# Performance work log

Measured on AMD Instinct MI355X. Metric: run time of the kernel, lower is better.

## Reference

```python
import jax, jax.numpy as jnp
import numpy as np

B, T, NUM_IN, H, O = 64, 128, 256, 512, 256
BANKS, N, M = 4, 128, 64
R = BANKS * N  # addressable memory rows (flattened over banks)
EPS = 1e-8


def _lin(key, out_d, in_d):
    s = 1.0 / np.sqrt(in_d)
    kw, kb = jax.random.split(key)
    W = jax.random.uniform(kw, (out_d, in_d), jnp.float32, -s, s)
    b = jax.random.uniform(kb, (out_d,), jnp.float32, -s, s)
    return W, b


def setup_inputs() -> dict:
    key = jax.random.key(0)
    ks = jax.random.split(key, 16)
    inp = {
        "x": jax.random.normal(ks[0], (B, T, 16, 16), jnp.float32),
        "h": jnp.zeros((B, H), jnp.float32),
        "frf": jnp.full((B, R), 1.0 / R, jnp.float32),
        "wrf": jnp.full((B, R), 1.0 / R, jnp.float32),
        "fwf": jnp.full((B, R), 1.0 / R, jnp.float32),
        "wwf": jnp.full((B, R), 1.0 / R, jnp.float32),
        "m": 0.1 * jax.random.normal(ks[1], (B, BANKS, N, M), jnp.float32),
    }
    inp["W_in"], inp["b_in"] = _lin(ks[2], H, NUM_IN)
    inp["W_read"], inp["b_read"] = _lin(ks[3], H, M)
    inp["W_out"], inp["b_out"] = _lin(ks[4], O, H)
    inp["W_kr"], inp["b_kr"] = _lin(ks[5], M, H)
    inp["W_br"], inp["b_br"] = _lin(ks[6], 1, H)
    inp["W_gr"], inp["b_gr"] = _lin(ks[7], 1, H)
    inp["W_kw"], inp["b_kw"] = _lin(ks[8], M, H)
    inp["W_bw"], inp["b_bw"] = _lin(ks[9], 1, H)
    inp["W_gw"], inp["b_gw"] = _lin(ks[10], 1, H)
    inp["W_e"], inp["b_e"] = _lin(ks[11], M, H)
    inp["W_a"], inp["b_a"] = _lin(ks[12], M, H)
    return inp


def _smooth(w):
    # wide filter: circular 3-tap blur of the focused filter over memory rows
    return 0.25 * jnp.roll(w, 1, axis=-1) + 0.5 * w + 0.25 * jnp.roll(w, -1, axis=-1)


def _address(h, mem2, f_prev, W_k, b_k, W_b, b_b, W_g, b_g):
    # content-based addressing with focused/wide filter pair (NTM-style)
    k = jnp.tanh(h @ W_k.T + b_k)                                  # [B,M]
    beta = jax.nn.softplus(h @ W_b.T + b_b)                        # [B,1]
    g = jax.nn.sigmoid(h @ W_g.T + b_g)                            # [B,1]
    dots = jnp.einsum("bm,brm->br", k, mem2)
    denom = (jnp.linalg.norm(k, axis=-1, keepdims=True)
             * jnp.linalg.norm(mem2, axis=-1) + EPS)
    wc = jax.nn.softmax(beta * dots / denom, axis=-1)              # [B,R]
    f_new = g * wc + (1.0 - g) * f_prev                            # focused filter
    w_new = _smooth(f_new)                                         # wide filter
    return f_new, w_new, 0.5 * (f_new + w_new)


def reference(x, h, frf, wrf, fwf, wwf, m,
              W_in, b_in, W_read, b_read, W_out, b_out,
              W_kr, b_kr, W_br, b_br, W_gr, b_gr,
              W_kw, b_kw, W_bw, b_bw, W_gw, b_gw,
              W_e, b_e, W_a, b_a):
    xs = x.transpose(1, 0, 2, 3).reshape(T, B, -1)  # [T,B,NUM_IN]

    def step(carry, x_t):
        h_t, frf_t, wrf_t, fwf_t, wwf_t, m_t = carry
        mem2 = m_t.reshape(B, R, M)
        # --- EMM read ---
        frf_n, wrf_n, w_read = _address(h_t, mem2, frf_t,
                                        W_kr, b_kr, W_br, b_br, W_gr, b_gr)
        r_t = jnp.einsum("br,brm->bm", w_read, mem2)               # [B,M]
        # --- EMM write ---
        fwf_n, wwf_n, w_write = _address(h_t, mem2, fwf_t,
                                         W_kw, b_kw, W_bw, b_bw, W_gw, b_gw)
        e = jax.nn.sigmoid(h_t @ W_e.T + b_e)                      # erase [B,M]
        a = jnp.tanh(h_t @ W_a.T + b_a)                            # add   [B,M]
        mem_new = (mem2 * (1.0 - w_write[:, :, None] * e[:, None, :])
                   + w_write[:, :, None] * a[:, None, :])
        m_n = mem_new.reshape(B, BANKS, N, M)
        # --- controller + output ---
        h_n = jax.nn.relu(x_t @ W_in.T + b_in + r_t @ W_read.T + b_read)
        out = jax.nn.sigmoid(h_n @ W_out.T + b_out)                # [B,O]
        return (h_n, frf_n, wrf_n, fwf_n, wwf_n, m_n), out

    _, outs = jax.lax.scan(step, (h, frf, wrf, fwf, wwf, m), xs)
    return outs.transpose(1, 0, 2)  # [B,T,O]
```

## Files before the change

### kernel.cpp

```cpp
#include <hip/hip_runtime.h>
#include <math.h>

#define B_   64
#define T_   128
#define NIN  256
#define H_   512
#define O_   256
#define M_   64
#define R_   512
#define EPS_ 1e-8f

typedef _Float16 h2 __attribute__((ext_vector_type(2)));

__device__ __forceinline__ float dot4(float4 a, float4 b) {
    return a.x*b.x + a.y*b.y + a.z*b.z + a.w*b.w;
}

__device__ __forceinline__ float frcp(float x) {
#if __has_builtin(__builtin_amdgcn_rcpf)
    return __builtin_amdgcn_rcpf(x);
#else
    return 1.f / x;
#endif
}
__device__ __forceinline__ float fsqrt_(float x) {
#if __has_builtin(__builtin_amdgcn_sqrtf)
    return __builtin_amdgcn_sqrtf(x);
#else
    return sqrtf(x);
#endif
}

__device__ __forceinline__ float fd2(unsigned wu, unsigned hu, float acc) {
#if __has_builtin(__builtin_amdgcn_fdot2)
    return __builtin_amdgcn_fdot2(__builtin_bit_cast(h2, wu),
                                  __builtin_bit_cast(h2, hu), acc, false);
#else
    h2 w = __builtin_bit_cast(h2, wu), h = __builtin_bit_cast(h2, hu);
    return acc + (float)w[0]*(float)h[0] + (float)w[1]*(float)h[1];
#endif
}
#define FD4(W, HX, A) { A = fd2(W.x, HX.x, A); A = fd2(W.y, HX.y, A); \
                        A = fd2(W.z, HX.z, A); A = fd2(W.w, HX.w, A); }

__device__ __forceinline__ unsigned pk16(float a, float b) {
    return __builtin_bit_cast(unsigned, __builtin_amdgcn_cvt_pkrtz(a, b));
}
__device__ __forceinline__ unsigned short bits16(float v) {
    return __builtin_bit_cast(unsigned short, (_Float16)v);
}

template<int CTRL>
__device__ __forceinline__ float dpp_add(float v) {
    int t = __builtin_amdgcn_update_dpp(0, __float_as_int(v), CTRL, 0xF, 0xF, false);
    return v + __int_as_float(t);
}
template<int CTRL>
__device__ __forceinline__ float dpp_mov(float v) {
    return __int_as_float(__builtin_amdgcn_update_dpp(0, __float_as_int(v), CTRL, 0xF, 0xF, false));
}
__device__ __forceinline__ float red16(float v) {
    v = dpp_add<0xB1>(v);
    v = dpp_add<0x4E>(v);
    v = dpp_add<0x124>(v);
    v = dpp_add<0x128>(v);
    return v;
}
__device__ __forceinline__ float red64_pair(float v) {
    v = dpp_add<0x4E>(v);
    v = dpp_add<0x124>(v);
    v = dpp_add<0x128>(v);
    v += __shfl_xor(v, 16, 64);
    v += __shfl_xor(v, 32, 64);
    return v;
}
__device__ __forceinline__ float sigmoid_f(float x) { return frcp(1.f + __expf(-x)); }
__device__ __forceinline__ float softplus_f(float x){ return x > 20.f ? x : log1pf(__expf(x)); }

__global__ __launch_bounds__(256) void w2h(
    const float* __restrict__ Wkr, const float* __restrict__ Wkw,
    const float* __restrict__ We,  const float* __restrict__ Wa,
    const float* __restrict__ Wbr, const float* __restrict__ Wgr,
    const float* __restrict__ Wbw, const float* __restrict__ Wgw,
    unsigned short* __restrict__ Wh)
{
    if (blockIdx.x == 128) {
        const int idx = threadIdx.x * 8;
        #pragma unroll
        for (int k = 0; k < 8; ++k) {
            int i2 = idx + k;
            int mi2 = i2 >> 9;
            const float* s2 = mi2 == 0 ? Wbr : mi2 == 1 ? Wgr : mi2 == 2 ? Wbw : Wgw;
            Wh[256 * H_ + i2] = bits16(s2[i2 & (H_ - 1)]);
        }
        return;
    }
    const int mi = blockIdx.x >> 5;
    const float* s = mi == 0 ? Wkr : mi == 1 ? Wkw : mi == 2 ? We : Wa;
    const int off = (blockIdx.x & 31) * 1024 + threadIdx.x * 4;
    float4 v = *(const float4*)&s[off];
    ushort4 o;
    o.x = bits16(v.x); o.y = bits16(v.y); o.z = bits16(v.z); o.w = bits16(v.w);
    *(ushort4*)&Wh[mi * 32768 + off] = o;
}

__global__ __launch_bounds__(256) void xin_gemm(
    const float* __restrict__ x, const float* __restrict__ Win,
    const float* __restrict__ bin, unsigned short* __restrict__ xin_h)
{
    __shared__ __align__(16) float xs[32 * NIN];
    const int tid  = threadIdx.x;
    const int row0 = blockIdx.x * 32;

    #pragma unroll
    for (int i = 0; i < 8; ++i) {
        int idx = i * 1024 + tid * 4;
        *(float4*)&xs[idx] = *(const float4*)&x[(size_t)row0 * NIN + idx];
    }
    __syncthreads();

    const int rg = tid >> 6;
    const int cg = tid & 63;
    const int c0 = cg * 8;
    float acc[8][8];
    #pragma unroll
    for (int r = 0; r < 8; ++r)
        #pragma unroll
        for (int c = 0; c < 8; ++c) acc[r][c] = 0.f;

    for (int k = 0; k < NIN; k += 4) {
        float4 xq[8];
        #pragma unroll
        for (int r = 0; r < 8; ++r) xq[r] = *(float4*)&xs[(rg * 8 + r) * NIN + k];
        #pragma unroll
        for (int c = 0; c < 8; ++c) {
            float4 w4 = *(const float4*)&Win[(size_t)(c0 + c) * NIN + k];
            #pragma unroll
            for (int r = 0; r < 8; ++r) acc[r][c] += dot4(xq[r], w4);
        }
    }
    #pragma unroll
    for (int r = 0; r < 8; ++r) {
        int grow = row0 + rg * 8 + r;
        ushort4 o0, o1;
        o0.x = bits16(acc[r][0] + bin[c0 + 0]);
        o0.y = bits16(acc[r][1] + bin[c0 + 1]);
        o0.z = bits16(acc[r][2] + bin[c0 + 2]);
        o0.w = bits16(acc[r][3] + bin[c0 + 3]);
        o1.x = bits16(acc[r][4] + bin[c0 + 4]);
        o1.y = bits16(acc[r][5] + bin[c0 + 5]);
        o1.z = bits16(acc[r][6] + bin[c0 + 6]);
        o1.w = bits16(acc[r][7] + bin[c0 + 7]);
        *(ushort4*)&xin_h[(size_t)grow * H_ + c0]     = o0;
        *(ushort4*)&xin_h[(size_t)grow * H_ + c0 + 4] = o1;
    }
}

__global__ __launch_bounds__(512, 2) void ntm_loop(
    const unsigned short* __restrict__ xin_h,
    const float* __restrict__ h0,
    const float* __restrict__ frf0, const float* __restrict__ fwf0,
    const float* __restrict__ m0,
    const unsigned short* __restrict__ Wh,
    const float* __restrict__ bkr_g, const float* __restrict__ bkw_g,
    const float* __restrict__ be_g,  const float* __restrict__ ba_g,
    const float* __restrict__ bbr_g, const float* __restrict__ bgr_g,
    const float* __restrict__ bbw_g, const float* __restrict__ bgw_g,
    const float* __restrict__ Wread, const float* __restrict__ bread_g,
    float* __restrict__ h_all)
{
    __shared__ __align__(16) unsigned short hh40[16 * 40];
    __shared__ __align__(16) unsigned wrh[R_ * 36];
    __shared__ __align__(16) float2 ffb[2][R_];
    __shared__ __align__(16) float2 dotsRW[R_];
    __shared__ __align__(16) float2 fwp[R_];
    __shared__ __align__(16) float proj4[4 * M_];
    __shared__ __align__(16) float rtp[8][M_];
    __shared__ __align__(16) float rt8[8][M_];
    __shared__ __align__(16) float2 wsumRW[16];
    __shared__ __align__(16) float bias256[4 * M_];
    __shared__ __align__(16) unsigned wheadu[4 * H_ / 2];
    __shared__ float bhead[4];
    __shared__ float scal[4];

    const int b    = blockIdx.x;
    const int tid  = threadIdx.x;
    const int wave = tid >> 6, lane = tid & 63;
    const int g    = lane >> 4, sub = lane & 15;
    const int group = tid >> 4, s16 = tid & 15;

    const float* mg = m0 + (size_t)b * (R_ * M_);
    float4 mreg[16];
    #pragma unroll
    for (int i = 0; i < 16; ++i)
        mreg[i] = *(const float4*)&mg[(wave * 64 + i * 4 + g) * M_ + sub * 4];

    uint4 w16[32];
    #pragma unroll
    for (int p = 0; p < 8; ++p)
        #pragma unroll
        for (int j = 0; j < 4; ++j)
            w16[p * 4 + j] = *(const uint4*)&Wh[(size_t)(p * 32 + group) * H_ + s16 * 32 + j * 8];

    hh40[(tid >> 5) * 40 + (tid & 31)] = bits16(h0[b * H_ + tid]);
    ffb[0][tid] = make_float2(frf0[b * R_ + tid], fwf0[b * R_ + tid]);
    if (tid < M_) {
        bias256[tid]          = bkr_g[tid];
        bias256[M_ + tid]     = bkw_g[tid];
        bias256[2 * M_ + tid] = be_g[tid];
        bias256[3 * M_ + tid] = ba_g[tid];
    }
    if (tid >= 8 && tid < 16) wsumRW[tid] = make_float2(0.f, 0.f);
    wheadu[tid * 2]     = ((const unsigned*)&Wh[256 * H_])[tid * 2];
    wheadu[tid * 2 + 1] = ((const unsigned*)&Wh[256 * H_])[tid * 2 + 1];
    if (tid < 4) bhead[tid] = (tid == 0 ? bbr_g : tid == 1 ? bgr_g : tid == 2 ? bbw_g : bgw_g)[0];

    {
        const float* wrp = Wread + (size_t)tid * M_;
        #pragma unroll
        for (int wd = 0; wd < 2; ++wd)
            #pragma unroll
            for (int c = 0; c < 4; ++c) {
                float4 wa = *(const float4*)&wrp[wd * 32 + c * 8];
                float4 wb = *(const float4*)&wrp[wd * 32 + c * 8 + 4];
                uint4 o;
                o.x = pk16(wa.x, wa.y); o.y = pk16(wa.z, wa.w);
                o.z = pk16(wb.x, wb.y); o.w = pk16(wb.z, wb.w);
                *(uint4*)&wrh[tid * 36 + wd * 16 + c * 4] = o;
            }
    }
    const float breg = bread_g[tid];
    __syncthreads();

    for (int t = 0; t < T_; ++t) {
        const int cur = t & 1, nxt = cur ^ 1;

        unsigned short xbits = xin_h[(size_t)(b * T_ + t) * H_ + tid];
        {
            uint4 hx0 = *(const uint4*)&hh40[s16 * 40 + 0];
            uint4 hx1 = *(const uint4*)&hh40[s16 * 40 + 8];
            uint4 hx2 = *(const uint4*)&hh40[s16 * 40 + 16];
            uint4 hx3 = *(const uint4*)&hh40[s16 * 40 + 24];
            float a[8];
            #pragma unroll
            for (int p = 0; p < 8; ++p) {
                float acc = 0.f;
                FD4(w16[p * 4 + 0], hx0, acc);
                FD4(w16[p * 4 + 1], hx1, acc);
                FD4(w16[p * 4 + 2], hx2, acc);
                FD4(w16[p * 4 + 3], hx3, acc);
                a[p] = red16(acc);
            }
            float av = a[0];
            #pragma unroll
            for (int p = 1; p < 8; ++p) av = (s16 == p) ? a[p] : av;
            const int rowp = (s16 & 7) * 32 + group;
            const int m = rowp >> 6;
            float xv = av + bias256[rowp];
            float e  = __expf((m == 2) ? -xv : 2.f * xv);
            float rcp = frcp(1.f + e);
            float act = (m == 2) ? rcp : 1.f - 2.f * rcp;
            if (s16 < 8) proj4[rowp] = act;

            if (wave == 0) {
                float a8 = 0.f;
                uint4 wh0 = *(const uint4*)&wheadu[group * 256 + s16 * 16 + 0];
                uint4 wh1 = *(const uint4*)&wheadu[group * 256 + s16 * 16 + 4];
                uint4 wh2 = *(const uint4*)&wheadu[group * 256 + s16 * 16 + 8];
                uint4 wh3 = *(const uint4*)&wheadu[group * 256 + s16 * 16 + 12];
                FD4(wh0, hx0, a8); FD4(wh1, hx1, a8);
                FD4(wh2, hx2, a8); FD4(wh3, hx3, a8);
                a8 = red16(a8);
                if (s16 == 0) {
                    float hv = a8 + bhead[group];
                    scal[group] = (group & 1) ? sigmoid_f(hv) : softplus_f(hv);
                }
            }
        }
        __syncthreads();

        {
            float4 kr4 = *(float4*)&proj4[sub * 4];
            float4 kw4 = *(float4*)&proj4[M_ + sub * 4];
            float snKR = fsqrt_(red16(dot4(kr4, kr4)));
            float snKW = fsqrt_(red16(dot4(kw4, kw4)));
            const bool isW = (sub == 1);
            float bta = isW ? scal[2] : scal[0];
            float snK = isW ? snKW : snKR;
            float eacc = 0.f;
            #pragma unroll
            for (int i = 0; i < 16; ++i) {
                int r = wave * 64 + i * 4 + g;
                float4 v = mreg[i];
                float c = dot4(kr4, v);
                float d = dot4(kw4, v);
                float n = dot4(v, v);
                float c2 = dpp_add<0xB1>(c), d2 = dpp_add<0xB1>(d), n2 = dpp_add<0xB1>(n);
                float c4 = dpp_add<0x4E>(c2), d4 = dpp_add<0x4E>(d2), n4 = dpp_add<0x4E>(n2);
                const int q = sub & 3;
                float z = (q == 0) ? c4 : (q == 1 ? d4 : n4);
                z = dpp_add<0x124>(z);
                z = dpp_add<0x128>(z);
                float nt = dpp_mov<0xAA>(z);
                float sn = fsqrt_(nt);
                float ee = __expf(bta * z * frcp(snK * sn + EPS_));
                float eo = dpp_mov<0xB1>(ee);
                if (sub == 0) dotsRW[r] = make_float2(ee, eo);
                eacc += (sub < 2) ? ee : 0.f;
            }
            float vsum = red64_pair(eacc);
            float vo = dpp_mov<0xB1>(vsum);
            if (lane == 0) wsumRW[wave] = make_float2(vsum, vo);
        }
        __syncthreads();

        {
            float2 ws = wsumRW[lane & 15];
            float totR = red16(ws.x);
            float totW = red16(ws.y);
            {
                const int r = wave * 64 + lane;
                float invR = frcp(totR), invW = frcp(totW);
                const int rm = (r + R_ - 1) & (R_ - 1), rp = (r + 1) & (R_ - 1);
                float gr = scal[1], gw = scal[3];
                float2 d0 = dotsRW[r];
                float2 dm = dotsRW[rm];
                float2 dp = dotsRW[rp];
                float2 p0 = ffb[cur][r];
                float2 pm = ffb[cur][rm];
                float2 pp = ffb[cur][rp];

                float f0 = gr * d0.x * invR + (1.f - gr) * p0.x;
                float fm = gr * dm.x * invR + (1.f - gr) * pm.x;
                float fp = gr * dp.x * invR + (1.f - gr) * pp.x;
                float q0 = gw * d0.y * invW + (1.f - gw) * p0.y;
                float qm = gw * dm.y * invW + (1.f - gw) * pm.y;
                float qp = gw * dp.y * invW + (1.f - gw) * pp.y;
                ffb[nxt][r] = make_float2(f0, q0);
                fwp[r] = make_float2(0.75f * f0 + 0.125f * (fm + fp),
                                     0.75f * q0 + 0.125f * (qm + qp));
            }
            __builtin_amdgcn_wave_barrier();

            float2 fw2[16];
            #pragma unroll
            for (int i = 0; i < 16; ++i)
                fw2[i] = fwp[wave * 64 + i * 4 + g];

            float4 e4 = *(float4*)&proj4[2 * M_ + sub * 4];
            float4 a4 = *(float4*)&proj4[3 * M_ + sub * 4];
            float rt0 = 0, rt1 = 0, rt2 = 0, rt3 = 0;
            #pragma unroll
            for (int i = 0; i < 16; ++i) {
                float wr = fw2[i].x, ww = fw2[i].y;
                float4 v = mreg[i];
                rt0 += wr * v.x; rt1 += wr * v.y; rt2 += wr * v.z; rt3 += wr * v.w;
                float4 nv;
                nv.x = v.x * (1.f - ww * e4.x) + ww * a4.x;
                nv.y = v.y * (1.f - ww * e4.y) + ww * a4.y;
                nv.z = v.z * (1.f - ww * e4.z) + ww * a4.z;
                nv.w = v.w * (1.f - ww * e4.w) + ww * a4.w;
                mreg[i] = nv;
            }
            rt0 += __shfl_xor(rt0, 16, 64); rt0 += __shfl_xor(rt0, 32, 64);
            rt1 += __shfl_xor(rt1, 16, 64); rt1 += __shfl_xor(rt1, 32, 64);
            rt2 += __shfl_xor(rt2, 16, 64); rt2 += __shfl_xor(rt2, 32, 64);
            rt3 += __shfl_xor(rt3, 16, 64); rt3 += __shfl_xor(rt3, 32, 64);
            if (g == 0)
                *(float4*)&rtp[wave][sub * 4] = make_float4(rt0, rt1, rt2, rt3);
        }
        __syncthreads();

        {
            float rsum = rtp[0][lane] + rtp[1][lane] + rtp[2][lane] + rtp[3][lane]
                       + rtp[4][lane] + rtp[5][lane] + rtp[6][lane] + rtp[7][lane];
            rt8[wave][lane] = rsum;
            __builtin_amdgcn_wave_barrier();

            float acc = 0.f;
            #pragma unroll
            for (int wd = 0; wd < 2; ++wd)
                #pragma unroll
                for (int c = 0; c < 4; ++c) {
                    uint4 wq = *(uint4*)&wrh[tid * 36 + wd * 16 + c * 4];
                    float4 ra = *(float4*)&rt8[wave][wd * 32 + c * 8];
                    float4 rb = *(float4*)&rt8[wave][wd * 32 + c * 8 + 4];
                    unsigned p0 = pk16(ra.x, ra.y), p1 = pk16(ra.z, ra.w);
                    unsigned p2 = pk16(rb.x, rb.y), p3 = pk16(rb.z, rb.w);
                    acc = fd2(wq.x, p0, acc); acc = fd2(wq.y, p1, acc);
                    acc = fd2(wq.z, p2, acc); acc = fd2(wq.w, p3, acc);
                }
            float xv = (float)__builtin_bit_cast(_Float16, xbits);
            float hv = fmaxf(xv + acc + breg, 0.f);
            hh40[(tid >> 5) * 40 + (tid & 31)] = bits16(hv);
            h_all[(size_t)(b * T_ + t) * H_ + tid] = hv;
        }
        __syncthreads();
    }
}

__global__ __launch_bounds__(256) void out_gemm(
    const float* __restrict__ h_all, const float* __restrict__ Wout,
    const float* __restrict__ bout, float* __restrict__ out)
{
    __shared__ __align__(16) float hs[32 * H_];
    const int tid  = threadIdx.x;
    const int row0 = blockIdx.x * 32;

    #pragma unroll
    for (int i = 0; i < 16; ++i) {
        int idx = i * 1024 + tid * 4;
        *(float4*)&hs[idx] = *(const float4*)&h_all[(size_t)row0 * H_ + idx];
    }
    __syncthreads();

    const int rg = tid >> 6;
    const int cg = tid & 63;
    const int c0 = cg * 4;
    float acc[8][4];
    #pragma unroll
    for (int r = 0; r < 8; ++r)
        #pragma unroll
        for (int c = 0; c < 4; ++c) acc[r][c] = 0.f;

    for (int k = 0; k < H_; k += 4) {
        float4 xq[8];
        #pragma unroll
        for (int r = 0; r < 8; ++r) xq[r] = *(float4*)&hs[(rg * 8 + r) * H_ + k];
        #pragma unroll
        for (int c = 0; c < 4; ++c) {
            float4 w4 = *(const float4*)&Wout[(size_t)(c0 + c) * H_ + k];
            #pragma unroll
            for (int r = 0; r < 8; ++r) acc[r][c] += dot4(xq[r], w4);
        }
    }
    #pragma unroll
    for (int r = 0; r < 8; ++r) {
        int grow = row0 + rg * 8 + r;
        float4 o4;
        o4.x = sigmoid_f(acc[r][0] + bout[c0 + 0]);
        o4.y = sigmoid_f(acc[r][1] + bout[c0 + 1]);
        o4.z = sigmoid_f(acc[r][2] + bout[c0 + 2]);
        o4.w = sigmoid_f(acc[r][3] + bout[c0 + 3]);
        *(float4*)&out[(size_t)grow * O_ + c0] = o4;
    }
}

extern "C" void kernel_launch(void* const* d_in, const int* in_sizes, int n_in,
                              void* d_out, int out_size, void* d_ws, size_t ws_size,
                              hipStream_t stream) {
    const float* x     = (const float*)d_in[0];
    const float* h0    = (const float*)d_in[1];
    const float* frf   = (const float*)d_in[2];
    const float* fwf   = (const float*)d_in[4];
    const float* m0    = (const float*)d_in[6];
    const float* Win   = (const float*)d_in[7];
    const float* bin   = (const float*)d_in[8];
    const float* Wread = (const float*)d_in[9];
    const float* bread = (const float*)d_in[10];
    const float* Wout  = (const float*)d_in[11];
    const float* bout  = (const float*)d_in[12];
    const float* Wkr   = (const float*)d_in[13];
    const float* bkr   = (const float*)d_in[14];
    const float* Wbr   = (const float*)d_in[15];
    const float* bbr   = (const float*)d_in[16];
    const float* Wgr   = (const float*)d_in[17];
    const float* bgr   = (const float*)d_in[18];
    const float* Wkw   = (const float*)d_in[19];
    const float* bkw   = (const float*)d_in[20];
    const float* Wbw   = (const float*)d_in[21];
    const float* bbw   = (const float*)d_in[22];
    const float* Wgw   = (const float*)d_in[23];
    const float* bgw   = (const float*)d_in[24];
    const float* We    = (const float*)d_in[25];
    const float* be    = (const float*)d_in[26];
    const float* Wa    = (const float*)d_in[27];
    const float* ba    = (const float*)d_in[28];

    unsigned short* xin_h = (unsigned short*)d_ws;
    float* h_all = (float*)((char*)d_ws + (size_t)B_ * T_ * H_ * 2);
    unsigned short* Wh = (unsigned short*)((char*)d_ws + (size_t)B_ * T_ * H_ * 6);

    w2h<<<129, 256, 0, stream>>>(Wkr, Wkw, We, Wa, Wbr, Wgr, Wbw, Wgw, Wh);
    xin_gemm<<<256, 256, 0, stream>>>(x, Win, bin, xin_h);
    ntm_loop<<<B_, 512, 0, stream>>>(xin_h, h0, frf, fwf, m0,
        Wh, bkr, bkw, be, ba,
        bbr, bgr, bbw, bgw,
        Wread, bread, h_all);
    out_gemm<<<256, 256, 0, stream>>>(h_all, Wout, bout, (float*)d_out);
}
```

Before: 900.9 us.

## Replace input and output FP32 GEMMs with FP16 MFMA matrix-core kernels

Adds a conversion kernel that casts x, W_in and W_out to half precision, then replaces the scalar FP32 xin and out GEMMs with one generic MFMA 16x16x32 f16 GEMM kernel. The recurrent loop now writes its hidden states in half precision instead of FP32, which halves that traffic and feeds the output GEMM directly. The goal is to move the two large batched GEMMs onto matrix cores. In exchange it adds an extra conversion pass over x, loses precision in h and x, and reads A and B straight from global memory without LDS staging.

```diff
diff --git a/kernel.cpp b/kernel.cpp
--- a/kernel.cpp
+++ b/kernel.cpp
@@ -11,6 +11,8 @@
 #define EPS_ 1e-8f
 
 typedef _Float16 h2 __attribute__((ext_vector_type(2)));
+typedef _Float16 f16x8 __attribute__((ext_vector_type(8)));
+typedef float f32x4 __attribute__((ext_vector_type(4)));
 
 __device__ __forceinline__ float dot4(float4 a, float4 b) {
     return a.x*b.x + a.y*b.y + a.z*b.z + a.w*b.w;
@@ -76,6 +78,23 @@
 }
 __device__ __forceinline__ float sigmoid_f(float x) { return frcp(1.f + __expf(-x)); }
 __device__ __forceinline__ float softplus_f(float x){ return x > 20.f ? x : log1pf(__expf(x)); }
+
+__global__ __launch_bounds__(256) void cvt_all(
+    const float* __restrict__ x, const float* __restrict__ Win,
+    const float* __restrict__ Wout,
+    unsigned short* __restrict__ xh, unsigned short* __restrict__ Winh,
+    unsigned short* __restrict__ Wouth)
+{
+    const int bid = blockIdx.x;
+    const float* src; unsigned short* dst; int idx;
+    if (bid < 2048)      { src = x;    dst = xh;    idx = bid * 1024 + threadIdx.x * 4; }
+    else if (bid < 2176) { src = Win;  dst = Winh;  idx = (bid - 2048) * 1024 + threadIdx.x * 4; }
+    else                 { src = Wout; dst = Wouth; idx = (bid - 2176) * 1024 + threadIdx.x * 4; }
+    float4 v = *(const float4*)&src[idx];
+    ushort4 o;
+    o.x = bits16(v.x); o.y = bits16(v.y); o.z = bits16(v.z); o.w = bits16(v.w);
+    *(ushort4*)&dst[idx] = o;
+}
 
 __global__ __launch_bounds__(256) void w2h(
     const float* __restrict__ Wkr, const float* __restrict__ Wkw,
@@ -104,55 +123,48 @@
     *(ushort4*)&Wh[mi * 32768 + off] = o;
 }
 
-__global__ __launch_bounds__(256) void xin_gemm(
-    const float* __restrict__ x, const float* __restrict__ Win,
-    const float* __restrict__ bin, unsigned short* __restrict__ xin_h)
+__global__ __launch_bounds__(256) void gemm_mfma(
+    const unsigned short* __restrict__ Ah, const unsigned short* __restrict__ Bh,
+    const float* __restrict__ bias, void* __restrict__ outp,
+    int M, int K, int N, int mode)
 {
-    __shared__ __align__(16) float xs[32 * NIN];
     const int tid  = threadIdx.x;
-    const int row0 = blockIdx.x * 32;
-
+    const int wv   = tid >> 6, lane = tid & 63;
+    const int m0   = blockIdx.x * 128 + wv * 32;
+    const int n0   = blockIdx.y * 64;
+    const int fr   = lane & 15, kg = lane >> 4;
+
+    f32x4 acc[2][4] = {};
+    const unsigned short* pa0 = Ah + (size_t)(m0 + fr) * K + kg * 8;
+    const unsigned short* pa1 = pa0 + (size_t)16 * K;
+    const unsigned short* pb  = Bh + (size_t)(n0 + fr) * K + kg * 8;
+
+    for (int k0 = 0; k0 < K; k0 += 32) {
+        f16x8 a0 = *(const f16x8*)(pa0 + k0);
+        f16x8 a1 = *(const f16x8*)(pa1 + k0);
+        #pragma unroll
+        for (int j = 0; j < 4; ++j) {
+            f16x8 bj = *(const f16x8*)(pb + (size_t)j * 16 * K + k0);
+            acc[0][j] = __builtin_amdgcn_mfma_f32_16x16x32_f16(a0, bj, acc[0][j], 0, 0, 0);
+            acc[1][j] = __builtin_amdgcn_mfma_f32_16x16x32_f16(a1, bj, acc[1][j], 0, 0, 0);
+        }
+    }
     #pragma unroll
-    for (int i = 0; i < 8; ++i) {
-        int idx = i * 1024 + tid * 4;
-        *(float4*)&xs[idx] = *(const float4*)&x[(size_t)row0 * NIN + idx];
-    }
-    __syncthreads();
-
-    const int rg = tid >> 6;
-    const int cg = tid & 63;
-    const int c0 = cg * 8;
-    float acc[8][8];
-    #pragma unroll
-    for (int r = 0; r < 8; ++r)
+    for (int j = 0; j < 4; ++j) {
+        const int gcol = n0 + j * 16 + fr;
+        const float bv = bias[gcol];
         #pragma unroll
-        for (int c = 0; c < 8; ++c) acc[r][c] = 0.f;
-
-    for (int k = 0; k < NIN; k += 4) {
-        float4 xq[8];
-        #pragma unroll
-        for (int r = 0; r < 8; ++r) xq[r] = *(float4*)&xs[(rg * 8 + r) * NIN + k];
-        #pragma unroll
-        for (int c = 0; c < 8; ++c) {
-            float4 w4 = *(const float4*)&Win[(size_t)(c0 + c) * NIN + k];
-            #pragma unroll
-            for (int r = 0; r < 8; ++r) acc[r][c] += dot4(xq[r], w4);
-        }
-    }
-    #pragma unroll
-    for (int r = 0; r < 8; ++r) {
-        int grow = row0 + rg * 8 + r;
-        ushort4 o0, o1;
-        o0.x = bits16(acc[r][0] + bin[c0 + 0]);
-        o0.y = bits16(acc[r][1] + bin[c0 + 1]);
-        o0.z = bits16(acc[r][2] + bin[c0 + 2]);
-        o0.w = bits16(acc[r][3] + bin[c0 + 3]);
-        o1.x = bits16(acc[r][4] + bin[c0 + 4]);
-        o1.y = bits16(acc[r][5] + bin[c0 + 5]);
-        o1.z = bits16(acc[r][6] + bin[c0 + 6]);
-        o1.w = bits16(acc[r][7] + bin[c0 + 7]);
-        *(ushort4*)&xin_h[(size_t)grow * H_ + c0]     = o0;
-        *(ushort4*)&xin_h[(size_t)grow * H_ + c0 + 4] = o1;
+        for (int i = 0; i < 2; ++i) {
+            #pragma unroll
+            for (int r = 0; r < 4; ++r) {
+                const int grow = m0 + i * 16 + kg * 4 + r;
+                float v = acc[i][j][r] + bv;
+                if (mode == 0)
+                    ((unsigned short*)outp)[(size_t)grow * N + gcol] = bits16(v);
+                else
+                    ((float*)outp)[(size_t)grow * N + gcol] = sigmoid_f(v);
+            }
+        }
     }
 }
 
@@ -167,7 +179,7 @@
     const float* __restrict__ bbr_g, const float* __restrict__ bgr_g,
     const float* __restrict__ bbw_g, const float* __restrict__ bgw_g,
     const float* __restrict__ Wread, const float* __restrict__ bread_g,
-    float* __restrict__ h_all)
+    unsigned short* __restrict__ h_all)
 {
     __shared__ __align__(16) unsigned short hh40[16 * 40];
     __shared__ __align__(16) unsigned wrh[R_ * 36];
@@ -392,57 +404,11 @@
                 }
             float xv = (float)__builtin_bit_cast(_Float16, xbits);
             float hv = fmaxf(xv + acc + breg, 0.f);
-            hh40[(tid >> 5) * 40 + (tid & 31)] = bits16(hv);
-            h_all[(size_t)(b * T_ + t) * H_ + tid] = hv;
+            unsigned short hb = bits16(hv);
+            hh40[(tid >> 5) * 40 + (tid & 31)] = hb;
+            h_all[(size_t)(b * T_ + t) * H_ + tid] = hb;
         }
         __syncthreads();
-    }
-}
-
-__global__ __launch_bounds__(256) void out_gemm(
-    const float* __restrict__ h_all, const float* __restrict__ Wout,
-    const float* __restrict__ bout, float* __restrict__ out)
-{
-    __shared__ __align__(16) float hs[32 * H_];
-    const int tid  = threadIdx.x;
-    const int row0 = blockIdx.x * 32;
-
-    #pragma unroll
-    for (int i = 0; i < 16; ++i) {
-        int idx = i * 1024 + tid * 4;
-        *(float4*)&hs[idx] = *(const float4*)&h_all[(size_t)row0 * H_ + idx];
-    }
-    __syncthreads();
-
-    const int rg = tid >> 6;
-    const int cg = tid & 63;
-    const int c0 = cg * 4;
-    float acc[8][4];
-    #pragma unroll
-    for (int r = 0; r < 8; ++r)
-        #pragma unroll
-        for (int c = 0; c < 4; ++c) acc[r][c] = 0.f;
-
-    for (int k = 0; k < H_; k += 4) {
-        float4 xq[8];
-        #pragma unroll
-        for (int r = 0; r < 8; ++r) xq[r] = *(float4*)&hs[(rg * 8 + r) * H_ + k];
-        #pragma unroll
-        for (int c = 0; c < 4; ++c) {
-            float4 w4 = *(const float4*)&Wout[(size_t)(c0 + c) * H_ + k];
-            #pragma unroll
-            for (int r = 0; r < 8; ++r) acc[r][c] += dot4(xq[r], w4);
-        }
-    }
-    #pragma unroll
-    for (int r = 0; r < 8; ++r) {
-        int grow = row0 + rg * 8 + r;
-        float4 o4;
-        o4.x = sigmoid_f(acc[r][0] + bout[c0 + 0]);
-        o4.y = sigmoid_f(acc[r][1] + bout[c0 + 1]);
-        o4.z = sigmoid_f(acc[r][2] + bout[c0 + 2]);
-        o4.w = sigmoid_f(acc[r][3] + bout[c0 + 3]);
-        *(float4*)&out[(size_t)grow * O_ + c0] = o4;
     }
 }
 
@@ -477,15 +443,22 @@
     const float* Wa    = (const float*)d_in[27];
     const float* ba    = (const float*)d_in[28];
 
-    unsigned short* xin_h = (unsigned short*)d_ws;
-    float* h_all = (float*)((char*)d_ws + (size_t)B_ * T_ * H_ * 2);
-    unsigned short* Wh = (unsigned short*)((char*)d_ws + (size_t)B_ * T_ * H_ * 6);
-
+    char* ws = (char*)d_ws;
+    unsigned short* xin_h  = (unsigned short*)(ws);
+    unsigned short* h_allh = (unsigned short*)(ws + (8u << 20));
+    unsigned short* Wh     = (unsigned short*)(ws + (16u << 20));
+    unsigned short* xh     = (unsigned short*)(ws + (17u << 20));
+    unsigned short* Winh   = (unsigned short*)(ws + (21u << 20));
+    unsigned short* Wouth  = (unsigned short*)(ws + (21u << 20) + (512u << 10));
+
+    cvt_all<<<2304, 256, 0, stream>>>(x, Win, Wout, xh, Winh, Wouth);
     w2h<<<129, 256, 0, stream>>>(Wkr, Wkw, We, Wa, Wbr, Wgr, Wbw, Wgw, Wh);
-    xin_gemm<<<256, 256, 0, stream>>>(x, Win, bin, xin_h);
+    gemm_mfma<<<dim3(B_ * T_ / 128, H_ / 64), 256, 0, stream>>>(
+        xh, Winh, bin, xin_h, B_ * T_, NIN, H_, 0);
     ntm_loop<<<B_, 512, 0, stream>>>(xin_h, h0, frf, fwf, m0,
         Wh, bkr, bkw, be, ba,
         bbr, bgr, bbw, bgw,
-        Wread, bread, h_all);
-    out_gemm<<<256, 256, 0, stream>>>(h_all, Wout, bout, (float*)d_out);
-}
+        Wread, bread, h_allh);
+    gemm_mfma<<<dim3(B_ * T_ / 128, O_ / 64), 256, 0, stream>>>(
+        h_allh, Wouth, bout, d_out, B_ * T_, H_, O_, 1);
+}
```

Result: faster. 792.4 us (-12.0%).
